# Kernel optimization log

Measured on AMD Instinct MI355X. Metric: run time of the kernel, lower is better.

Reference implementation:

```python
import jax, jax.numpy as jnp
import numpy as np

DIM = 2048
HEADS = 16
DIM_HEAD = 128
ROPE_THETA = 10000.0


def _rope(t):
    # t: [b, h, n, d]; lucidrains rotary-embedding-torch style (interleaved pairs)
    n, d = t.shape[-2], t.shape[-1]
    inv_freq = 1.0 / (ROPE_THETA ** (jnp.arange(0, d, 2, dtype=jnp.float32) / d))  # [d/2]
    freqs = jnp.arange(n, dtype=jnp.float32)[:, None] * inv_freq[None, :]          # [n, d/2]
    freqs = jnp.repeat(freqs, 2, axis=-1)                                          # [n, d]
    cos, sin = jnp.cos(freqs), jnp.sin(freqs)
    x1 = t[..., 0::2]
    x2 = t[..., 1::2]
    rot = jnp.stack((-x2, x1), axis=-1).reshape(t.shape)  # rotate_half on interleaved pairs
    return t * cos + rot * sin


def setup_inputs() -> dict:
    key = jax.random.key(0)
    k1, k2, k3 = jax.random.split(key, 3)
    x = jax.random.normal(k1, (2, 2048, DIM), dtype=jnp.float32)
    gamma = jnp.ones((DIM,), dtype=jnp.float32)
    w_qkv = jax.random.normal(k2, (DIM, 3 * HEADS * DIM_HEAD), dtype=jnp.float32) * 0.02
    w_out = jax.random.normal(k3, (HEADS * DIM_HEAD, DIM), dtype=jnp.float32) * 0.02
    return {"x": x, "gamma": gamma, "w_qkv": w_qkv, "w_out": w_out}


def reference(x, gamma, w_qkv, w_out):
    b, n, dim = x.shape
    # RMSNorm: F.normalize(x, dim=-1) * sqrt(dim) * gamma
    norm = jnp.linalg.norm(x, axis=-1, keepdims=True)
    xn = x / jnp.maximum(norm, 1e-12) * (dim ** 0.5) * gamma
    # QKV projection; 'b n (qkv h d) -> qkv b h n d'
    qkv = (xn @ w_qkv).reshape(b, n, 3, HEADS, DIM_HEAD).transpose(2, 0, 3, 1, 4)
    q, k, v = qkv[0], qkv[1], qkv[2]
    cached_kv = jnp.stack((k, v))  # [2, b, h, n, d] (pre-RoPE, as in original)
    q = _rope(q)
    k = _rope(k)
    sim = jnp.einsum('bhid,bhjd->bhij', q, k) * (DIM_HEAD ** -0.5)
    causal_mask = jnp.triu(jnp.ones((n, n), dtype=bool), 1)
    sim = jnp.where(causal_mask, -jnp.finfo(sim.dtype).max, sim)
    attn = jax.nn.softmax(sim, axis=-1)
    out = jnp.einsum('bhij,bhjd->bhid', attn, v)
    out = out.transpose(0, 2, 1, 3).reshape(b, n, HEADS * DIM_HEAD)
    out = out @ w_out
    return (out, cached_kv)
```

## Files before the change

### kernel.cpp

```cpp
#include <hip/hip_runtime.h>
#include <cstdint>
#include <cstddef>
#include <math.h>

#define SEQ   2048
#define DIM   2048
#define NQKV  6144
#define NH    16
#define DH    128
#define ROWS  4096

typedef unsigned short u16;
typedef unsigned int u32;
typedef __attribute__((ext_vector_type(8))) short bf16x8;
typedef __attribute__((ext_vector_type(4))) float f32x4;
typedef __attribute__((ext_vector_type(16))) float f32x16;

__device__ __forceinline__ u16 f2bf(float f) {
  union { float f; u32 u; } v;
  v.f = f;
  u32 r = v.u + 0x7FFFu + ((v.u >> 16) & 1u);
  return (u16)(r >> 16);
}

__device__ __forceinline__ void gll16(const u16* g, u16* l) {
  __builtin_amdgcn_global_load_lds(
      (const __attribute__((address_space(1))) u32*)(const void*)g,
      (__attribute__((address_space(3))) u32*)(void*)l,
      16, 0, 0);
}

__global__ __launch_bounds__(64) void rms_slow(
    const float* __restrict__ x, const float* __restrict__ g,
    float* __restrict__ xn) {
  int row = blockIdx.x, lane = threadIdx.x;
  const float* xr = x + (size_t)row * DIM;
  double ss = 0.0;
  for (int c = lane; c < DIM; c += 64) { double v = xr[c]; ss += v * v; }
  #pragma unroll
  for (int off = 32; off >= 1; off >>= 1) ss += __shfl_xor(ss, off);
  double nrm = sqrt(ss); if (nrm < 1e-12) nrm = 1e-12;
  double sc = 45.254833995939045 / nrm;
  float* dst = xn + (size_t)row * DIM;
  for (int c = lane; c < DIM; c += 64) dst[c] = (float)((double)xr[c] * sc * (double)g[c]);
}

__global__ __launch_bounds__(256) void cast_bf16(
    const float* __restrict__ in, u16* __restrict__ out) {
  size_t i = ((size_t)blockIdx.x * 256 + threadIdx.x) * 8;
  float4 f0 = *(const float4*)(in + i);
  float4 f1 = *(const float4*)(in + i + 4);
  union { u16 h[8]; int4 q; } cv;
  cv.h[0]=f2bf(f0.x); cv.h[1]=f2bf(f0.y); cv.h[2]=f2bf(f0.z); cv.h[3]=f2bf(f0.w);
  cv.h[4]=f2bf(f1.x); cv.h[5]=f2bf(f1.y); cv.h[6]=f2bf(f1.z); cv.h[7]=f2bf(f1.w);
  *(int4*)(out + i) = cv.q;
}

__global__ void transpose_f32_bf16(const float* __restrict__ in,
                                   u16* __restrict__ out, int R, int C) {
  __shared__ float tile[32][33];
  int bx = blockIdx.x * 32;
  int by = blockIdx.y * 32;
  int tx = threadIdx.x, ty = threadIdx.y;
  #pragma unroll
  for (int j = 0; j < 32; j += 8)
    tile[ty + j][tx] = in[(size_t)(by + ty + j) * C + bx + tx];
  __syncthreads();
  #pragma unroll
  for (int j = 0; j < 32; j += 8)
    out[(size_t)(bx + ty + j) * R + by + tx] = f2bf(tile[tx][ty + j]);
}

__global__ __launch_bounds__(256) void gemm_nt(
    const u16* __restrict__ A, const u16* __restrict__ BT,
    float* __restrict__ C, int M, int N, int K) {
  __shared__ u16 As[128 * 32];
  __shared__ u16 Bs[128 * 32];
  int nbn = N >> 7;
  int chunk = nbn >> 3;
  int wg = blockIdx.x;
  int xcd = wg & 7, g = wg >> 3;
  int bm = (g / chunk) * 128;
  int bn = (xcd * chunk + g % chunk) * 128;

  int tid = threadIdx.x;
  int wid = tid >> 6, lane = tid & 63;
  int wr = wid >> 1, wc = wid & 1;
  int fr = lane & 15, fq = lane >> 4;
  int srow_hi = lane >> 2;
  int scol = (lane & 3) * 8;

  f32x4 acc[4][4] = {};

  const u16* a_rd = As + (wr * 64 + fr) * 32 + fq * 8;
  const u16* b_rd = Bs + (wc * 64 + fr) * 32 + fq * 8;

  for (int k0 = 0; k0 < K; k0 += 32) {
    __syncthreads();
    #pragma unroll
    for (int i = 0; i < 2; ++i) {
      int c = wid * 2 + i;
      int row = c * 16 + srow_hi;
      gll16(A  + (size_t)(bm + row) * K + k0 + scol, As + c * 512);
      gll16(BT + (size_t)(bn + row) * K + k0 + scol, Bs + c * 512);
    }
    __syncthreads();

    bf16x8 af[4], bfr[4];
    #pragma unroll
    for (int m = 0; m < 4; ++m) af[m]  = *(const bf16x8*)(a_rd + m * 16 * 32);
    #pragma unroll
    for (int n = 0; n < 4; ++n) bfr[n] = *(const bf16x8*)(b_rd + n * 16 * 32);
    #pragma unroll
    for (int m = 0; m < 4; ++m)
      #pragma unroll
      for (int n = 0; n < 4; ++n)
        acc[m][n] = __builtin_amdgcn_mfma_f32_16x16x32_bf16(af[m], bfr[n], acc[m][n], 0, 0, 0);
  }
  #pragma unroll
  for (int m = 0; m < 4; ++m)
    #pragma unroll
    for (int n = 0; n < 4; ++n)
      #pragma unroll
      for (int r = 0; r < 4; ++r) {
        int row = bm + wr * 64 + m * 16 + fq * 4 + r;
        int col = bn + wc * 64 + n * 16 + fr;
        C[(size_t)row * N + col] = acc[m][n][r];
      }
}

__global__ __launch_bounds__(256) void rope_table(float2* __restrict__ tab) {
  int gid = blockIdx.x * 256 + threadIdx.x;
  int p = gid & 63;
  int n = gid >> 6;
  double inv = pow(10000.0, -(double)p / 64.0);
  double ang = (double)n * inv;
  tab[gid] = make_float2((float)cos(ang), (float)sin(ang));
}

__global__ void transpose_v_cast(const float* __restrict__ qkv,
                                 u16* __restrict__ vT) {
  int bh = blockIdx.z; int b = bh >> 4, h = bh & 15;
  int d0 = blockIdx.x * 32, n0 = blockIdx.y * 32;
  __shared__ float tile[32][33];
  int tx = threadIdx.x, ty = threadIdx.y;
  const float* src = qkv + (size_t)(b * SEQ + n0) * NQKV + 2 * DIM + h * DH + d0;
  #pragma unroll
  for (int j = 0; j < 32; j += 8)
    tile[ty + j][tx] = src[(size_t)(ty + j) * NQKV + tx];
  __syncthreads();
  u16* dst = vT + ((size_t)bh * DH + d0) * SEQ + n0;
  #pragma unroll
  for (int j = 0; j < 32; j += 8)
    dst[(size_t)(ty + j) * SEQ + tx] = f2bf(tile[tx][ty + j]);
}

__global__ __launch_bounds__(256) void kv_rope_pack(
    float* __restrict__ qkv, float* __restrict__ cached,
    const float2* __restrict__ tab) {
  int row = blockIdx.x;
  int b = row >> 11, n = row & 2047;
  int t = threadIdx.x;
  int c = t * 8;
  int h = c >> 7, d = c & 127;
  float* base = qkv + (size_t)row * NQKV;

  float4 q0 = *(const float4*)(base + c);
  float4 q1 = *(const float4*)(base + c + 4);
  float4 k0 = *(const float4*)(base + 2048 + c);
  float4 k1 = *(const float4*)(base + 2048 + c + 4);
  float4 v0 = *(const float4*)(base + 4096 + c);
  float4 v1 = *(const float4*)(base + 4096 + c + 4);

  size_t ob = ((size_t)(b * NH + h) * SEQ + n) * DH + d;
  *(float4*)(cached + ob)     = k0;
  *(float4*)(cached + ob + 4) = k1;
  *(float4*)(cached + 8388608 + ob)     = v0;
  *(float4*)(cached + 8388608 + ob + 4) = v1;

  int p0 = d >> 1;
  float2 cs0 = tab[n * 64 + p0];
  float2 cs1 = tab[n * 64 + p0 + 1];
  float2 cs2 = tab[n * 64 + p0 + 2];
  float2 cs3 = tab[n * 64 + p0 + 3];

  float qa0 = q0.x * cs0.x - q0.y * cs0.y, qb0 = q0.y * cs0.x + q0.x * cs0.y;
  float qa1 = q0.z * cs1.x - q0.w * cs1.y, qb1 = q0.w * cs1.x + q0.z * cs1.y;
  float qa2 = q1.x * cs2.x - q1.y * cs2.y, qb2 = q1.y * cs2.x + q1.x * cs2.y;
  float qa3 = q1.z * cs3.x - q1.w * cs3.y, qb3 = q1.w * cs3.x + q1.z * cs3.y;

  float ka0 = k0.x * cs0.x - k0.y * cs0.y, kb0 = k0.y * cs0.x + k0.x * cs0.y;
  float ka1 = k0.z * cs1.x - k0.w * cs1.y, kb1 = k0.w * cs1.x + k0.z * cs1.y;
  float ka2 = k1.x * cs2.x - k1.y * cs2.y, kb2 = k1.y * cs2.x + k1.x * cs2.y;
  float ka3 = k1.z * cs3.x - k1.w * cs3.y, kb3 = k1.w * cs3.x + k1.z * cs3.y;

  union { u16 hh[8]; int4 q; } pq, pk;
  pq.hh[0]=f2bf(qa0); pq.hh[1]=f2bf(qb0); pq.hh[2]=f2bf(qa1); pq.hh[3]=f2bf(qb1);
  pq.hh[4]=f2bf(qa2); pq.hh[5]=f2bf(qb2); pq.hh[6]=f2bf(qa3); pq.hh[7]=f2bf(qb3);
  pk.hh[0]=f2bf(ka0); pk.hh[1]=f2bf(kb0); pk.hh[2]=f2bf(ka1); pk.hh[3]=f2bf(kb1);
  pk.hh[4]=f2bf(ka2); pk.hh[5]=f2bf(kb2); pk.hh[6]=f2bf(ka3); pk.hh[7]=f2bf(kb3);

  __syncthreads();

  u16* ub = (u16*)base;
  *(int4*)(ub + 8192 + c)  = pq.q;
  *(int4*)(ub + 10240 + c) = pk.q;
}

__global__ __launch_bounds__(64) void attn_swap(
    const u16* __restrict__ qkp,
    const u16* __restrict__ vT,
    u16* __restrict__ ctx) {
  int wg = blockIdx.x;
  int xcd = wg & 7;
  int g   = wg >> 3;
  int bh  = (g >> 5) * 8 + xcd;
  int qp  = g & 31;
  int b = bh >> 4, h = bh & 15;
  int lane = threadIdx.x;
  int ln = lane & 31;
  int hi = lane >> 5;

  const size_t rstr = 2 * NQKV;
  const u16* Qb = qkp + (size_t)(b * SEQ) * rstr + 8192 + h * 128;
  const u16* Kb = qkp + (size_t)(b * SEQ) * rstr + 10240 + h * 128;
  const u16* Vt = vT + (size_t)bh * DH * SEQ;
  const float scale = 0.08838834764831845f;

  #pragma unroll 1
  for (int ph = 0; ph < 2; ++ph) {
    int qt = ph ? (63 - qp) : qp;
    int qr0 = qt * 32;
    int q_own = qr0 + ln;

    bf16x8 qf[8];
    {
      const u16* qrow = Qb + (size_t)q_own * rstr + hi * 8;
      #pragma unroll
      for (int kc = 0; kc < 8; ++kc) qf[kc] = *(const bf16x8*)(qrow + kc * 16);
    }

    f32x16 acc[4] = {};
    float m = -3e38f, l = 0.f;

    bf16x8 kreg[8];
    {
      const u16* krow = Kb + (size_t)ln * rstr + hi * 8;
      #pragma unroll
      for (int kc = 0; kc < 8; ++kc) kreg[kc] = *(const bf16x8*)(krow + kc * 16);
    }

    for (int jt = 0; jt <= qt; ++jt) {
      int j0 = jt * 32;

      bf16x8 vfrag[8];
      #pragma unroll
      for (int t = 0; t < 2; ++t)
        #pragma unroll
        for (int db = 0; db < 4; ++db)
          vfrag[t * 4 + db] =
              *(const bf16x8*)(Vt + (size_t)(db * 32 + ln) * SEQ + j0 + t * 16 + hi * 8);

      f32x16 sacc0 = {}, sacc1 = {};
      __builtin_amdgcn_s_setprio(1);
      #pragma unroll
      for (int kc = 0; kc < 4; ++kc)
        sacc0 = __builtin_amdgcn_mfma_f32_32x32x16_bf16(kreg[kc], qf[kc], sacc0, 0, 0, 0);
      #pragma unroll
      for (int kc = 4; kc < 8; ++kc)
        sacc1 = __builtin_amdgcn_mfma_f32_32x32x16_bf16(kreg[kc], qf[kc], sacc1, 0, 0, 0);
      __builtin_amdgcn_s_setprio(0);
      f32x16 sacc = sacc0 + sacc1;

      if (jt < qt) {
        const u16* krow = Kb + (size_t)(j0 + 32 + ln) * rstr + hi * 8;
        #pragma unroll
        for (int kc = 0; kc < 8; ++kc) kreg[kc] = *(const bf16x8*)(krow + kc * 16);
      }

      float p[16];
      #pragma unroll
      for (int r = 0; r < 16; ++r) {
        int kv = j0 + (r & 3) + 8 * (r >> 2) + 4 * hi;
        float v = sacc[r] * scale;
        p[r] = (kv > q_own) ? -1e30f : v;
      }

      float t8[8];
      #pragma unroll
      for (int i = 0; i < 8; ++i) t8[i] = fmaxf(p[i], p[i + 8]);
      #pragma unroll
      for (int i = 0; i < 4; ++i) t8[i] = fmaxf(t8[i], t8[i + 4]);
      float mx = fmaxf(fmaxf(t8[0], t8[1]), fmaxf(t8[2], t8[3]));
      mx = fmaxf(mx, __shfl_xor(mx, 32));

      if (!__all(mx - m <= 8.f)) {
        float mn = fmaxf(m, mx);
        float al = __expf(m - mn);
        m = mn;
        l *= al;
        #pragma unroll
        for (int r = 0; r < 16; ++r) {
          float alr = __shfl(al, (r & 3) + 8 * (r >> 2) + 4 * hi);
          #pragma unroll
          for (int db = 0; db < 4; ++db) acc[db][r] *= alr;
        }
      }

      #pragma unroll
      for (int r = 0; r < 16; ++r) p[r] = __expf(p[r] - m);
      float s8[8];
      #pragma unroll
      for (int i = 0; i < 8; ++i) s8[i] = p[i] + p[i + 8];
      #pragma unroll
      for (int i = 0; i < 4; ++i) s8[i] = s8[i] + s8[i + 4];
      float sum = (s8[0] + s8[1]) + (s8[2] + s8[3]);
      sum += __shfl_xor(sum, 32);
      l += sum;

      u32 pk[8], swk[8];
      #pragma unroll
      for (int i = 0; i < 8; ++i)
        pk[i] = (u32)f2bf(p[2 * i]) | ((u32)f2bf(p[2 * i + 1]) << 16);
      #pragma unroll
      for (int i = 0; i < 8; ++i) swk[i] = __shfl_xor(pk[i], 32);

      union { u32 w[4]; bf16x8 v; } pf0, pf1;
      pf0.w[0] = hi ? swk[2] : pk[0];
      pf0.w[1] = hi ? swk[3] : pk[1];
      pf0.w[2] = hi ? pk[2]  : swk[0];
      pf0.w[3] = hi ? pk[3]  : swk[1];
      pf1.w[0] = hi ? swk[6] : pk[4];
      pf1.w[1] = hi ? swk[7] : pk[5];
      pf1.w[2] = hi ? pk[6]  : swk[4];
      pf1.w[3] = hi ? pk[7]  : swk[5];

      __builtin_amdgcn_s_setprio(1);
      #pragma unroll
      for (int db = 0; db < 4; ++db) {
        acc[db] = __builtin_amdgcn_mfma_f32_32x32x16_bf16(pf0.v, vfrag[db],     acc[db], 0, 0, 0);
        acc[db] = __builtin_amdgcn_mfma_f32_32x32x16_bf16(pf1.v, vfrag[4 + db], acc[db], 0, 0, 0);
      }
      __builtin_amdgcn_s_setprio(0);
    }

    float linv = 1.f / l;
    #pragma unroll
    for (int r = 0; r < 16; ++r) {
      int qrow = (r & 3) + 8 * (r >> 2) + 4 * hi;
      float lr = __shfl(linv, qrow);
      int q = qr0 + qrow;
      u16* crow = ctx + (size_t)(b * SEQ + q) * DIM + h * DH + ln;
      #pragma unroll
      for (int db = 0; db < 4; ++db)
        crow[db * 32] = f2bf(acc[db][r] * lr);
    }
  }
}

extern "C" void kernel_launch(void* const* d_in, const int* in_sizes, int n_in,
                              void* d_out, int out_size, void* d_ws, size_t ws_size,
                              hipStream_t stream) {
  const float *x = nullptr, *gamma = nullptr, *wq = nullptr, *wo = nullptr;
  for (int ii = 0; ii < n_in; ++ii) {
    switch (in_sizes[ii]) {
      case  8388608: x     = (const float*)d_in[ii]; break;
      case     2048: gamma = (const float*)d_in[ii]; break;
      case 12582912: wq    = (const float*)d_in[ii]; break;
      case  4194304: wo    = (const float*)d_in[ii]; break;
    }
  }
  if (!x || !gamma || !wq || !wo) {
    x = (const float*)d_in[0]; gamma = (const float*)d_in[1];
    wq = (const float*)d_in[2]; wo = (const float*)d_in[3];
  }

  float* out    = (float*)d_out;
  float* cached = out + 8388608;

  float* xn    = (float*)d_ws;
  u16*   wqkvT = (u16*)d_ws;
  u16*   ctx   = (u16*)d_ws;
  u16*   woutT = (u16*)((char*)d_ws + 25165824);
  float* qkvf  = (float*)((char*)d_ws + 33554432);
  u16*   xnb   = (u16*)d_out;
  u16*   vT    = (u16*)d_out;
  float2* tab  = (float2*)((char*)d_out + 16777216);

  rms_slow<<<ROWS, 64, 0, stream>>>(x, gamma, xn);
  rope_table<<<131072 / 256, 256, 0, stream>>>(tab);
  cast_bf16<<<4096, 256, 0, stream>>>(xn, xnb);
  transpose_f32_bf16<<<dim3(NQKV / 32, DIM / 32), dim3(32, 8), 0, stream>>>(wq, wqkvT, DIM, NQKV);
  transpose_f32_bf16<<<dim3(DIM / 32, DIM / 32), dim3(32, 8), 0, stream>>>(wo, woutT, DIM, DIM);
  gemm_nt<<<(ROWS / 128) * (NQKV / 128), 256, 0, stream>>>(xnb, wqkvT, qkvf, ROWS, NQKV, DIM);
  transpose_v_cast<<<dim3(DH / 32, SEQ / 32, 32), dim3(32, 8), 0, stream>>>(qkvf, vT);
  kv_rope_pack<<<ROWS, 256, 0, stream>>>(qkvf, cached, tab);
  attn_swap<<<1024, 64, 0, stream>>>((const u16*)qkvf, vT, ctx);
  gemm_nt<<<(ROWS / 128) * (DIM / 128), 256, 0, stream>>>(ctx, woutT, out, ROWS, DIM, DIM);
}
```

Baseline: 425.4 us.

## Fuse RoPE, bf16 pack and KV cache write into QKV GEMM epilogue

Folds the bf16 cast into the RMSNorm kernel. Replaces the separate kv_rope_pack pass with a QKV GEMM epilogue that applies RoPE via a lane shuffle, writes bf16 Q/K into a compact buffer, and scatters the fp32 K/V cache directly. V goes to a dedicated fp32 buffer for the transpose. This removes a full fp32 QKV round trip and two launches. The cost is scattered, non-vectorized epilogue stores and per-element table loads inside the GEMM.

```diff
diff --git a/kernel.cpp b/kernel.cpp
--- a/kernel.cpp
+++ b/kernel.cpp
@@ -30,9 +30,9 @@
       16, 0, 0);
 }
 
-__global__ __launch_bounds__(64) void rms_slow(
+__global__ __launch_bounds__(64) void rms_bf16(
     const float* __restrict__ x, const float* __restrict__ g,
-    float* __restrict__ xn) {
+    u16* __restrict__ xnb) {
   int row = blockIdx.x, lane = threadIdx.x;
   const float* xr = x + (size_t)row * DIM;
   double ss = 0.0;
@@ -41,19 +41,9 @@
   for (int off = 32; off >= 1; off >>= 1) ss += __shfl_xor(ss, off);
   double nrm = sqrt(ss); if (nrm < 1e-12) nrm = 1e-12;
   double sc = 45.254833995939045 / nrm;
-  float* dst = xn + (size_t)row * DIM;
-  for (int c = lane; c < DIM; c += 64) dst[c] = (float)((double)xr[c] * sc * (double)g[c]);
-}
-
-__global__ __launch_bounds__(256) void cast_bf16(
-    const float* __restrict__ in, u16* __restrict__ out) {
-  size_t i = ((size_t)blockIdx.x * 256 + threadIdx.x) * 8;
-  float4 f0 = *(const float4*)(in + i);
-  float4 f1 = *(const float4*)(in + i + 4);
-  union { u16 h[8]; int4 q; } cv;
-  cv.h[0]=f2bf(f0.x); cv.h[1]=f2bf(f0.y); cv.h[2]=f2bf(f0.z); cv.h[3]=f2bf(f0.w);
-  cv.h[4]=f2bf(f1.x); cv.h[5]=f2bf(f1.y); cv.h[6]=f2bf(f1.z); cv.h[7]=f2bf(f1.w);
-  *(int4*)(out + i) = cv.q;
+  u16* dst = xnb + (size_t)row * DIM;
+  for (int c = lane; c < DIM; c += 64)
+    dst[c] = f2bf((float)((double)xr[c] * sc * (double)g[c]));
 }
 
 __global__ void transpose_f32_bf16(const float* __restrict__ in,
@@ -69,6 +59,15 @@
   #pragma unroll
   for (int j = 0; j < 32; j += 8)
     out[(size_t)(bx + ty + j) * R + by + tx] = f2bf(tile[tx][ty + j]);
+}
+
+__global__ __launch_bounds__(256) void rope_table(float2* __restrict__ tab) {
+  int gid = blockIdx.x * 256 + threadIdx.x;
+  int p = gid & 63;
+  int n = gid >> 6;
+  double inv = pow(10000.0, -(double)p / 64.0);
+  double ang = (double)n * inv;
+  tab[gid] = make_float2((float)cos(ang), (float)sin(ang));
 }
 
 __global__ __launch_bounds__(256) void gemm_nt(
@@ -129,82 +128,112 @@
       }
 }
 
-__global__ __launch_bounds__(256) void rope_table(float2* __restrict__ tab) {
-  int gid = blockIdx.x * 256 + threadIdx.x;
-  int p = gid & 63;
-  int n = gid >> 6;
-  double inv = pow(10000.0, -(double)p / 64.0);
-  double ang = (double)n * inv;
-  tab[gid] = make_float2((float)cos(ang), (float)sin(ang));
-}
-
-__global__ void transpose_v_cast(const float* __restrict__ qkv,
+__global__ __launch_bounds__(256) void gemm_qkv(
+    const u16* __restrict__ A, const u16* __restrict__ BT,
+    float* __restrict__ cached, u16* __restrict__ qpk,
+    float* __restrict__ vbuf, const float2* __restrict__ tab) {
+  const int M = ROWS, N = NQKV, K = DIM;
+  __shared__ u16 As[128 * 32];
+  __shared__ u16 Bs[128 * 32];
+  int nbn = N >> 7;
+  int chunk = nbn >> 3;
+  int wg = blockIdx.x;
+  int xcd = wg & 7, g = wg >> 3;
+  int bm = (g / chunk) * 128;
+  int bn = (xcd * chunk + g % chunk) * 128;
+
+  int tid = threadIdx.x;
+  int wid = tid >> 6, lane = tid & 63;
+  int wr = wid >> 1, wc = wid & 1;
+  int fr = lane & 15, fq = lane >> 4;
+  int srow_hi = lane >> 2;
+  int scol = (lane & 3) * 8;
+
+  f32x4 acc[4][4] = {};
+
+  const u16* a_rd = As + (wr * 64 + fr) * 32 + fq * 8;
+  const u16* b_rd = Bs + (wc * 64 + fr) * 32 + fq * 8;
+
+  for (int k0 = 0; k0 < K; k0 += 32) {
+    __syncthreads();
+    #pragma unroll
+    for (int i = 0; i < 2; ++i) {
+      int c = wid * 2 + i;
+      int row = c * 16 + srow_hi;
+      gll16(A  + (size_t)(bm + row) * K + k0 + scol, As + c * 512);
+      gll16(BT + (size_t)(bn + row) * K + k0 + scol, Bs + c * 512);
+    }
+    __syncthreads();
+
+    bf16x8 af[4], bfr[4];
+    #pragma unroll
+    for (int m = 0; m < 4; ++m) af[m]  = *(const bf16x8*)(a_rd + m * 16 * 32);
+    #pragma unroll
+    for (int n = 0; n < 4; ++n) bfr[n] = *(const bf16x8*)(b_rd + n * 16 * 32);
+    #pragma unroll
+    for (int m = 0; m < 4; ++m)
+      #pragma unroll
+      for (int n = 0; n < 4; ++n)
+        acc[m][n] = __builtin_amdgcn_mfma_f32_16x16x32_bf16(af[m], bfr[n], acc[m][n], 0, 0, 0);
+  }
+
+  int typ = bn >> 11;
+  if (typ < 2) {
+    #pragma unroll
+    for (int m = 0; m < 4; ++m)
+      #pragma unroll
+      for (int nn = 0; nn < 4; ++nn)
+        #pragma unroll
+        for (int r = 0; r < 4; ++r) {
+          int gr = bm + wr * 64 + m * 16 + fq * 4 + r;
+          int gc = bn + wc * 64 + nn * 16 + fr;
+          int n = gr & 2047;
+          int lc = gc & 2047;
+          int d = lc & 127;
+          float v = acc[m][nn][r];
+          float w = __shfl_xor(v, 1);
+          float2 cs = tab[n * 64 + (d >> 1)];
+          float o = (d & 1) ? (v * cs.x + w * cs.y) : (v * cs.x - w * cs.y);
+          qpk[(size_t)gr * 4096 + typ * 2048 + lc] = f2bf(o);
+          if (typ == 1) {
+            int b = gr >> 11, h = lc >> 7;
+            cached[((size_t)(b * NH + h) * SEQ + n) * DH + d] = v;
+          }
+        }
+  } else {
+    #pragma unroll
+    for (int m = 0; m < 4; ++m)
+      #pragma unroll
+      for (int nn = 0; nn < 4; ++nn)
+        #pragma unroll
+        for (int r = 0; r < 4; ++r) {
+          int gr = bm + wr * 64 + m * 16 + fq * 4 + r;
+          int gc = bn + wc * 64 + nn * 16 + fr;
+          int n = gr & 2047, b = gr >> 11;
+          int lc = gc - 4096;
+          int d = lc & 127, h = lc >> 7;
+          float v = acc[m][nn][r];
+          cached[8388608 + ((size_t)(b * NH + h) * SEQ + n) * DH + d] = v;
+          vbuf[(size_t)gr * 2048 + lc] = v;
+        }
+  }
+}
+
+__global__ void transpose_v_cast(const float* __restrict__ vbuf,
                                  u16* __restrict__ vT) {
   int bh = blockIdx.z; int b = bh >> 4, h = bh & 15;
   int d0 = blockIdx.x * 32, n0 = blockIdx.y * 32;
   __shared__ float tile[32][33];
   int tx = threadIdx.x, ty = threadIdx.y;
-  const float* src = qkv + (size_t)(b * SEQ + n0) * NQKV + 2 * DIM + h * DH + d0;
+  const float* src = vbuf + (size_t)(b * SEQ + n0) * 2048 + h * DH + d0;
   #pragma unroll
   for (int j = 0; j < 32; j += 8)
-    tile[ty + j][tx] = src[(size_t)(ty + j) * NQKV + tx];
+    tile[ty + j][tx] = src[(size_t)(ty + j) * 2048 + tx];
   __syncthreads();
   u16* dst = vT + ((size_t)bh * DH + d0) * SEQ + n0;
   #pragma unroll
   for (int j = 0; j < 32; j += 8)
     dst[(size_t)(ty + j) * SEQ + tx] = f2bf(tile[tx][ty + j]);
-}
-
-__global__ __launch_bounds__(256) void kv_rope_pack(
-    float* __restrict__ qkv, float* __restrict__ cached,
-    const float2* __restrict__ tab) {
-  int row = blockIdx.x;
-  int b = row >> 11, n = row & 2047;
-  int t = threadIdx.x;
-  int c = t * 8;
-  int h = c >> 7, d = c & 127;
-  float* base = qkv + (size_t)row * NQKV;
-
-  float4 q0 = *(const float4*)(base + c);
-  float4 q1 = *(const float4*)(base + c + 4);
-  float4 k0 = *(const float4*)(base + 2048 + c);
-  float4 k1 = *(const float4*)(base + 2048 + c + 4);
-  float4 v0 = *(const float4*)(base + 4096 + c);
-  float4 v1 = *(const float4*)(base + 4096 + c + 4);
-
-  size_t ob = ((size_t)(b * NH + h) * SEQ + n) * DH + d;
-  *(float4*)(cached + ob)     = k0;
-  *(float4*)(cached + ob + 4) = k1;
-  *(float4*)(cached + 8388608 + ob)     = v0;
-  *(float4*)(cached + 8388608 + ob + 4) = v1;
-
-  int p0 = d >> 1;
-  float2 cs0 = tab[n * 64 + p0];
-  float2 cs1 = tab[n * 64 + p0 + 1];
-  float2 cs2 = tab[n * 64 + p0 + 2];
-  float2 cs3 = tab[n * 64 + p0 + 3];
-
-  float qa0 = q0.x * cs0.x - q0.y * cs0.y, qb0 = q0.y * cs0.x + q0.x * cs0.y;
-  float qa1 = q0.z * cs1.x - q0.w * cs1.y, qb1 = q0.w * cs1.x + q0.z * cs1.y;
-  float qa2 = q1.x * cs2.x - q1.y * cs2.y, qb2 = q1.y * cs2.x + q1.x * cs2.y;
-  float qa3 = q1.z * cs3.x - q1.w * cs3.y, qb3 = q1.w * cs3.x + q1.z * cs3.y;
-
-  float ka0 = k0.x * cs0.x - k0.y * cs0.y, kb0 = k0.y * cs0.x + k0.x * cs0.y;
-  float ka1 = k0.z * cs1.x - k0.w * cs1.y, kb1 = k0.w * cs1.x + k0.z * cs1.y;
-  float ka2 = k1.x * cs2.x - k1.y * cs2.y, kb2 = k1.y * cs2.x + k1.x * cs2.y;
-  float ka3 = k1.z * cs3.x - k1.w * cs3.y, kb3 = k1.w * cs3.x + k1.z * cs3.y;
-
-  union { u16 hh[8]; int4 q; } pq, pk;
-  pq.hh[0]=f2bf(qa0); pq.hh[1]=f2bf(qb0); pq.hh[2]=f2bf(qa1); pq.hh[3]=f2bf(qb1);
-  pq.hh[4]=f2bf(qa2); pq.hh[5]=f2bf(qb2); pq.hh[6]=f2bf(qa3); pq.hh[7]=f2bf(qb3);
-  pk.hh[0]=f2bf(ka0); pk.hh[1]=f2bf(kb0); pk.hh[2]=f2bf(ka1); pk.hh[3]=f2bf(kb1);
-  pk.hh[4]=f2bf(ka2); pk.hh[5]=f2bf(kb2); pk.hh[6]=f2bf(ka3); pk.hh[7]=f2bf(kb3);
-
-  __syncthreads();
-
-  u16* ub = (u16*)base;
-  *(int4*)(ub + 8192 + c)  = pq.q;
-  *(int4*)(ub + 10240 + c) = pk.q;
 }
 
 __global__ __launch_bounds__(64) void attn_swap(
@@ -221,9 +250,9 @@
   int ln = lane & 31;
   int hi = lane >> 5;
 
-  const size_t rstr = 2 * NQKV;
-  const u16* Qb = qkp + (size_t)(b * SEQ) * rstr + 8192 + h * 128;
-  const u16* Kb = qkp + (size_t)(b * SEQ) * rstr + 10240 + h * 128;
+  const size_t rstr = 4096;
+  const u16* Qb = qkp + (size_t)(b * SEQ) * rstr + h * 128;
+  const u16* Kb = Qb + 2048;
   const u16* Vt = vT + (size_t)bh * DH * SEQ;
   const float scale = 0.08838834764831845f;
 
@@ -378,23 +407,22 @@
   float* out    = (float*)d_out;
   float* cached = out + 8388608;
 
-  float* xn    = (float*)d_ws;
-  u16*   wqkvT = (u16*)d_ws;
-  u16*   ctx   = (u16*)d_ws;
-  u16*   woutT = (u16*)((char*)d_ws + 25165824);
-  float* qkvf  = (float*)((char*)d_ws + 33554432);
-  u16*   xnb   = (u16*)d_out;
+  char* ws = (char*)d_ws;
+  u16*   xnb   = (u16*)ws;
+  u16*   qpk   = (u16*)(ws + 16777216);
+  float* vbuf  = (float*)(ws + 50331648);
+  u16*   wqkvT = (u16*)(ws + 83886080);
+  u16*   woutT = (u16*)(ws + 109051904);
+  u16*   ctx   = (u16*)(ws + 117440512);
   u16*   vT    = (u16*)d_out;
   float2* tab  = (float2*)((char*)d_out + 16777216);
 
-  rms_slow<<<ROWS, 64, 0, stream>>>(x, gamma, xn);
+  rms_bf16<<<ROWS, 64, 0, stream>>>(x, gamma, xnb);
   rope_table<<<131072 / 256, 256, 0, stream>>>(tab);
-  cast_bf16<<<4096, 256, 0, stream>>>(xn, xnb);
   transpose_f32_bf16<<<dim3(NQKV / 32, DIM / 32), dim3(32, 8), 0, stream>>>(wq, wqkvT, DIM, NQKV);
   transpose_f32_bf16<<<dim3(DIM / 32, DIM / 32), dim3(32, 8), 0, stream>>>(wo, woutT, DIM, DIM);
-  gemm_nt<<<(ROWS / 128) * (NQKV / 128), 256, 0, stream>>>(xnb, wqkvT, qkvf, ROWS, NQKV, DIM);
-  transpose_v_cast<<<dim3(DH / 32, SEQ / 32, 32), dim3(32, 8), 0, stream>>>(qkvf, vT);
-  kv_rope_pack<<<ROWS, 256, 0, stream>>>(qkvf, cached, tab);
-  attn_swap<<<1024, 64, 0, stream>>>((const u16*)qkvf, vT, ctx);
+  gemm_qkv<<<(ROWS / 128) * (NQKV / 128), 256, 0, stream>>>(xnb, wqkvT, cached, qpk, vbuf, tab);
+  transpose_v_cast<<<dim3(DH / 32, SEQ / 32, 32), dim3(32, 8), 0, stream>>>(vbuf, vT);
+  attn_swap<<<1024, 64, 0, stream>>>(qpk, vT, ctx);
   gemm_nt<<<(ROWS / 128) * (DIM / 128), 256, 0, stream>>>(ctx, woutT, out, ROWS, DIM, DIM);
 }
```

Measured after the change: 414.1 us. -2.7%, faster.
